# Kernel tuning notes

Hardware: AMD Instinct MI355X
Metric: run time of the kernel (lower is better)

Reference implementation:

```python
import jax, jax.numpy as jnp
import numpy as np

NUM_HEADS = 32
NUM_KV_HEADS = 8
HEAD_DIM = 128
EPS = 1e-6
ROPE_THETA = 10000.0


def setup_inputs() -> dict:
    key = jax.random.key(0)
    k1, k2, k3 = jax.random.split(key, 3)
    B, S, H = 2, 2048, 4096
    qkv_out = (NUM_HEADS + 2 * NUM_KV_HEADS) * HEAD_DIM  # 6144
    return {
        "hidden_states": jax.random.normal(k1, (B, S, H), dtype=jnp.float32),
        "positions": jnp.arange(S, dtype=jnp.int32),
        "wqkv": jax.random.normal(k2, (qkv_out, H), dtype=jnp.float32) * 0.02,
        "q_norm_w": jnp.ones((HEAD_DIM,), dtype=jnp.float32),
        "k_norm_w": jnp.ones((HEAD_DIM,), dtype=jnp.float32),
        "wo": jax.random.normal(k3, (H, H), dtype=jnp.float32) * 0.02,
    }


def _rmsnorm(x, w, eps=EPS):
    # per-head RMSNorm over last dim (head_dim), computed in fp32
    xf = x.astype(jnp.float32)
    var = jnp.mean(xf * xf, axis=-1, keepdims=True)
    return (xf * jax.lax.rsqrt(var + eps) * w).astype(x.dtype)


def _rope(x, positions):
    # NeoX-style half rotation, rotary_dim == head_dim
    d = x.shape[-1]
    half = d // 2
    inv_freq = 1.0 / (ROPE_THETA ** (jnp.arange(0, half, dtype=jnp.float32) * 2.0 / d))
    ang = positions.astype(jnp.float32)[:, None] * inv_freq[None, :]  # [S, half]
    cos = jnp.cos(ang)[None, :, None, :]  # [1,S,1,half]
    sin = jnp.sin(ang)[None, :, None, :]
    x1, x2 = x[..., :half], x[..., half:]
    return jnp.concatenate([x1 * cos - x2 * sin, x2 * cos + x1 * sin], axis=-1)


def reference(hidden_states, positions, wqkv, q_norm_w, k_norm_w, wo):
    B, S, H = hidden_states.shape
    scale = HEAD_DIM ** -0.5
    qkv = jnp.einsum("bsh,oh->bso", hidden_states, wqkv)
    q_size = NUM_HEADS * HEAD_DIM
    kv_size = NUM_KV_HEADS * HEAD_DIM
    q = qkv[..., :q_size].reshape(B, S, NUM_HEADS, HEAD_DIM)
    k = qkv[..., q_size:q_size + kv_size].reshape(B, S, NUM_KV_HEADS, HEAD_DIM)
    v = qkv[..., q_size + kv_size:].reshape(B, S, NUM_KV_HEADS, HEAD_DIM)
    q = _rmsnorm(q, q_norm_w)
    k = _rmsnorm(k, k_norm_w)
    q = _rope(q, positions)
    k = _rope(k, positions)
    # GQA: expand kv heads to query heads
    group = NUM_HEADS // NUM_KV_HEADS
    k = jnp.repeat(k, group, axis=2)  # [B,S,NUM_HEADS,D]
    v = jnp.repeat(v, group, axis=2)
    scores = jnp.einsum("bqhd,bkhd->bhqk", q, k) * scale
    causal = jnp.tril(jnp.ones((S, S), dtype=bool))
    scores = jnp.where(causal[None, None], scores, jnp.finfo(scores.dtype).min)
    probs = jax.nn.softmax(scores, axis=-1)
    attn = jnp.einsum("bhqk,bkhd->bqhd", probs, v).reshape(B, S, NUM_HEADS * HEAD_DIM)
    return jnp.einsum("bsi,oi->bso", attn, wo)
```

## Files before the change

### kernel.cpp

```cpp
#include <hip/hip_runtime.h>
#include <hip/hip_bf16.h>
#include <cstdint>
#include <cstddef>

typedef __hip_bfloat16 bf16;
typedef __attribute__((ext_vector_type(8))) short s8v;
typedef __attribute__((ext_vector_type(4))) float f4v;

#define NH 32
#define NKV 8
#define HD 128
#define BB 2
#define SS 2048
#define HH 4096
#define QKVO 6144
#define MM 4096

__device__ __forceinline__ void gld_lds16(const void* g, void* l) {
    __builtin_amdgcn_global_load_lds(
        (const __attribute__((address_space(1))) void*)g,
        (__attribute__((address_space(3))) void*)l, 16, 0, 0);
}

struct alignas(16) bf16x8s { bf16 v[8]; };
__global__ __launch_bounds__(256) void conv_kernel(const float* __restrict__ in,
                                                   bf16* __restrict__ out, int n8) {
    int i = blockIdx.x * 256 + threadIdx.x;
    if (i >= n8) return;
    const float4* in4 = (const float4*)in;
    float4 a = in4[i * 2];
    float4 b = in4[i * 2 + 1];
    bf16x8s p;
    p.v[0] = __float2bfloat16(a.x); p.v[1] = __float2bfloat16(a.y);
    p.v[2] = __float2bfloat16(a.z); p.v[3] = __float2bfloat16(a.w);
    p.v[4] = __float2bfloat16(b.x); p.v[5] = __float2bfloat16(b.y);
    p.v[6] = __float2bfloat16(b.z); p.v[7] = __float2bfloat16(b.w);
    *(bf16x8s*)(out + (size_t)i * 8) = p;
}

template <typename OutT>
__global__ __launch_bounds__(256) void gemm_bt(const bf16* __restrict__ A,
                                               const bf16* __restrict__ Bm,
                                               OutT* __restrict__ C,
                                               int M, int N, int K) {
    __shared__ bf16 sA[128 * 32];
    __shared__ bf16 sB[128 * 32];
    const int tid = threadIdx.x;
    const int lane = tid & 63;
    const int wave = tid >> 6;
    const int l15 = lane & 15, quad = lane >> 4;
    const int wm = (wave >> 1) * 64, wn = (wave & 1) * 64;
    const int bm = blockIdx.x, bn = blockIdx.y;
    const int row = tid >> 2;
    const int col8 = (tid & 3) * 8;
    const bf16* Ag = A + (size_t)(bm * 128 + row) * K + col8;
    const bf16* Bg = Bm + (size_t)(bn * 128 + row) * K + col8;

    f4v acc[4][4] = {};
    for (int kt = 0; kt < K; kt += 32) {
        __syncthreads();
        gld_lds16(Ag + kt, (char*)sA + tid * 16);
        gld_lds16(Ag + (size_t)64 * K + kt, (char*)sA + 4096 + tid * 16);
        gld_lds16(Bg + kt, (char*)sB + tid * 16);
        gld_lds16(Bg + (size_t)64 * K + kt, (char*)sB + 4096 + tid * 16);
        __syncthreads();
        s8v af[4], bfr[4];
#pragma unroll
        for (int mt = 0; mt < 4; mt++)
            af[mt] = *(const s8v*)(sA + (wm + mt * 16 + l15) * 32 + quad * 8);
#pragma unroll
        for (int nt = 0; nt < 4; nt++)
            bfr[nt] = *(const s8v*)(sB + (wn + nt * 16 + l15) * 32 + quad * 8);
#pragma unroll
        for (int mt = 0; mt < 4; mt++)
#pragma unroll
            for (int nt = 0; nt < 4; nt++)
                acc[mt][nt] = __builtin_amdgcn_mfma_f32_16x16x32_bf16(
                    af[mt], bfr[nt], acc[mt][nt], 0, 0, 0);
    }
#pragma unroll
    for (int mt = 0; mt < 4; mt++)
#pragma unroll
        for (int nt = 0; nt < 4; nt++) {
            int r0 = bm * 128 + wm + mt * 16 + quad * 4;
            int c0 = bn * 128 + wn + nt * 16 + l15;
#pragma unroll
            for (int r = 0; r < 4; r++) {
                float v = acc[mt][nt][r];
                if constexpr (sizeof(OutT) == 2)
                    C[(size_t)(r0 + r) * N + c0] = (OutT)__float2bfloat16(v);
                else
                    C[(size_t)(r0 + r) * N + c0] = (OutT)v;
            }
        }
}

__global__ __launch_bounds__(128) void norm_rope_kernel(
    const bf16* __restrict__ qkv, const int* __restrict__ positions,
    const float* __restrict__ qw, const float* __restrict__ kw,
    bf16* __restrict__ qb, bf16* __restrict__ kb) {
    int rowid = blockIdx.x;
    int head = blockIdx.y;
    int d = threadIdx.x;
    int b = rowid >> 11, s = rowid & 2047;
    bool isq = head < NH;
    int col = isq ? head * HD + d : NH * HD + (head - NH) * HD + d;
    float x = __bfloat162float(qkv[(size_t)rowid * QKVO + col]);

    __shared__ float sv[128];
    __shared__ float partial[2];
    float ss = x * x;
#pragma unroll
    for (int off = 32; off; off >>= 1) ss += __shfl_xor(ss, off, 64);
    if ((threadIdx.x & 63) == 0) partial[threadIdx.x >> 6] = ss;
    __syncthreads();
    float var = (partial[0] + partial[1]) * (1.0f / 128.0f);
    float w = isq ? qw[d] : kw[d];
    float xn = x * rsqrtf(var + 1e-6f) * w;
    sv[d] = xn;
    __syncthreads();

    float pos = (float)positions[s];
    float o;
    if (d < 64) {
        float ang = pos * exp2f(-(float)d * 0.20762051f);
        float c, si; __sincosf(ang, &si, &c);
        o = xn * c - sv[d + 64] * si;
    } else {
        int i = d - 64;
        float ang = pos * exp2f(-(float)i * 0.20762051f);
        float c, si; __sincosf(ang, &si, &c);
        o = xn * c + sv[i] * si;
    }
    if (isq) o *= 0.08838834764831845f;
    size_t oidx;
    if (isq) oidx = (((size_t)(b * NH + head) * SS + s) * HD + d);
    else     oidx = (((size_t)(b * NKV + (head - NH)) * SS + s) * HD + d);
    (isq ? qb : kb)[oidx] = __float2bfloat16(o);
}

__global__ __launch_bounds__(256) void vtrans_kernel(const bf16* __restrict__ qkv,
                                                     bf16* __restrict__ vt) {
    int bh = blockIdx.z;
    int s0 = blockIdx.x * 32, d0 = blockIdx.y * 32;
    int b = bh >> 3, hv = bh & 7;
    __shared__ bf16 tile[32][33];
    int tx = threadIdx.x, ty = threadIdx.y;
    size_t colbase = (size_t)(NH + NKV) * HD + hv * HD + d0;
    for (int i = 0; i < 4; i++) {
        int s = s0 + ty + i * 8;
        tile[ty + i * 8][tx] = qkv[(size_t)(b * SS + s) * QKVO + colbase + tx];
    }
    __syncthreads();
    for (int i = 0; i < 4; i++) {
        int d = d0 + ty + i * 8;
        vt[((size_t)(bh * HD + d)) * SS + s0 + tx] = tile[tx][ty + i * 8];
    }
}

__global__ __launch_bounds__(512, 4) void attn_kernel(
    const bf16* __restrict__ q, const bf16* __restrict__ k,
    const bf16* __restrict__ vt, bf16* __restrict__ out) {
    int pi = blockIdx.x;
    int h = blockIdx.y;
    int b = blockIdx.z;
    int hk = h >> 2;
    int tid = threadIdx.x, lane = tid & 63, wave = tid >> 6;
    int l15 = lane & 15, quad = lane >> 4;

    __shared__ bf16 sK[64][136];
    __shared__ bf16 sVt[128][72];
    __shared__ bf16 sP[8][16][72];

    const bf16* qg = q + ((size_t)(b * NH + h) * SS) * HD;
    const bf16* kg = k + ((size_t)(b * NKV + hk) * SS) * HD;
    const bf16* vg = vt + ((size_t)(b * NKV + hk) * HD) * SS;

    for (int half = 0; half < 2; half++) {
        int qt = half ? (15 - pi) : pi;
        int q0 = qt * 128;
        int qrow = q0 + wave * 16 + l15;
        s8v qf[4];
#pragma unroll
        for (int kc = 0; kc < 4; kc++)
            qf[kc] = *(const s8v*)(qg + (size_t)qrow * HD + kc * 32 + quad * 8);

        f4v o[8] = {};
        float lp[4] = {0.f, 0.f, 0.f, 0.f};
        int qgrow[4];
#pragma unroll
        for (int r = 0; r < 4; r++) qgrow[r] = q0 + wave * 16 + quad * 4 + r;

        int nkt = 2 * qt + 2;
        for (int kt = 0; kt < nkt; kt++) {
            int kbase = kt * 64;
            __syncthreads();
#pragma unroll
            for (int it = 0; it < 2; it++) {
                int c = tid + it * 512;
                int r = c >> 4, c8 = (c & 15) * 8;
                *(float4*)(&sK[r][c8]) =
                    *(const float4*)(kg + (size_t)(kbase + r) * HD + c8);
            }
#pragma unroll
            for (int it = 0; it < 2; it++) {
                int c = tid + it * 512;
                int dr = c >> 3, ck = (c & 7) * 8;
                *(float4*)(&sVt[dr][ck]) =
                    *(const float4*)(vg + (size_t)dr * SS + kbase + ck);
            }
            __syncthreads();

            f4v sc[4];
#pragma unroll
            for (int nt = 0; nt < 4; nt++) {
                f4v a = {0.f, 0.f, 0.f, 0.f};
#pragma unroll
                for (int kc = 0; kc < 4; kc++) {
                    s8v bfrag = *(const s8v*)(&sK[nt * 16 + l15][kc * 32 + quad * 8]);
                    a = __builtin_amdgcn_mfma_f32_16x16x32_bf16(qf[kc], bfrag, a, 0, 0, 0);
                }
                sc[nt] = a;
            }
#pragma unroll
            for (int nt = 0; nt < 4; nt++) {
                int kcol = kbase + nt * 16 + l15;
#pragma unroll
                for (int r = 0; r < 4; r++) {
                    float pv = (kcol > qgrow[r]) ? 0.f : __expf(sc[nt][r]);
                    sc[nt][r] = pv;
                    lp[r] += pv;
                }
            }
#pragma unroll
            for (int nt = 0; nt < 4; nt++)
#pragma unroll
                for (int r = 0; r < 4; r++)
                    sP[wave][quad * 4 + r][nt * 16 + l15] = __float2bfloat16(sc[nt][r]);
            asm volatile("s_waitcnt lgkmcnt(0)" ::: "memory");
            s8v pa[2];
#pragma unroll
            for (int kc = 0; kc < 2; kc++)
                pa[kc] = *(const s8v*)(&sP[wave][l15][kc * 32 + quad * 8]);
#pragma unroll
            for (int dt = 0; dt < 8; dt++)
#pragma unroll
                for (int kc = 0; kc < 2; kc++) {
                    s8v vb = *(const s8v*)(&sVt[dt * 16 + l15][kc * 32 + quad * 8]);
                    o[dt] = __builtin_amdgcn_mfma_f32_16x16x32_bf16(pa[kc], vb, o[dt], 0, 0, 0);
                }
        }
#pragma unroll
        for (int off = 1; off < 16; off <<= 1)
#pragma unroll
            for (int r = 0; r < 4; r++) lp[r] += __shfl_xor(lp[r], off, 64);
#pragma unroll
        for (int r = 0; r < 4; r++) {
            float inv = 1.0f / lp[r];
            int sg = qgrow[r];
#pragma unroll
            for (int dt = 0; dt < 8; dt++) {
                int d = dt * 16 + l15;
                out[(((size_t)(b * SS + sg)) * NH + h) * HD + d] =
                    __float2bfloat16(o[dt][r] * inv);
            }
        }
    }
}

extern "C" void kernel_launch(void* const* d_in, const int* in_sizes, int n_in,
                              void* d_out, int out_size, void* d_ws, size_t ws_size,
                              hipStream_t stream) {
    const float* hidden = (const float*)d_in[0];
    const int* positions = (const int*)d_in[1];
    const float* wqkv = (const float*)d_in[2];
    const float* qnw = (const float*)d_in[3];
    const float* knw = (const float*)d_in[4];
    const float* wo = (const float*)d_in[5];
    float* out = (float*)d_out;

    char* ws = (char*)d_ws;
    bf16* hid_bf = (bf16*)ws;
    bf16* wbuf   = (bf16*)(ws + 33554432);
    bf16* qkv    = (bf16*)(ws + 33554432 + 50331648);
    bf16* qb     = (bf16*)(ws + 33554432 + 50331648 + 50331648);
    bf16* kb     = (bf16*)(ws + 33554432 + 50331648 + 50331648 + 33554432);
    bf16* vtb    = (bf16*)(ws + 33554432 + 50331648 + 50331648 + 33554432 + 8388608);
    bf16* attn   = qkv;

    conv_kernel<<<2097152 / 256, 256, 0, stream>>>(hidden, hid_bf, 2097152);
    conv_kernel<<<3145728 / 256, 256, 0, stream>>>(wqkv, wbuf, 3145728);
    gemm_bt<bf16><<<dim3(32, 48), 256, 0, stream>>>(hid_bf, wbuf, qkv, MM, QKVO, HH);
    norm_rope_kernel<<<dim3(4096, 40), 128, 0, stream>>>(qkv, positions, qnw, knw, qb, kb);
    vtrans_kernel<<<dim3(64, 4, 16), dim3(32, 8), 0, stream>>>(qkv, vtb);
    attn_kernel<<<dim3(8, 32, 2), 512, 0, stream>>>(qb, kb, vtb, attn);
    conv_kernel<<<2097152 / 256, 256, 0, stream>>>(wo, wbuf, 2097152);
    gemm_bt<float><<<dim3(32, 32), 256, 0, stream>>>(attn, wbuf, out, MM, HH, HH);
}
```

Before: 864.2 us.

## Replace GEMM with 256x256 double-buffered swizzled-LDS pipelined MFMA kernel

Replaces the simple 128x128 single-buffered GEMM with a 256x256-tile, 512-thread kernel. It uses double-buffered LDS, XOR-swizzled shared layout, split-phase async global-to-LDS staging interleaved with MFMA blocks, s_setprio, and workgroup index swizzling for L2 locality. The goal is to hide load latency, raise arithmetic intensity, and cut LDS bank conflicts in both projection GEMMs. In exchange it uses 128KB of LDS and many more registers, and the hand-placed waitcnt counts are fragile.

```diff
diff --git a/kernel.cpp b/kernel.cpp
--- a/kernel.cpp
+++ b/kernel.cpp
@@ -21,6 +21,8 @@
         (const __attribute__((address_space(1))) void*)g,
         (__attribute__((address_space(3))) void*)l, 16, 0, 0);
 }
+
+#define MFMA_BF16(a, b, c) __builtin_amdgcn_mfma_f32_16x16x32_bf16((a), (b), (c), 0, 0, 0)
 
 struct alignas(16) bf16x8s { bf16 v[8]; };
 __global__ __launch_bounds__(256) void conv_kernel(const float* __restrict__ in,
@@ -38,55 +40,139 @@
     *(bf16x8s*)(out + (size_t)i * 8) = p;
 }
 
+__device__ __forceinline__ void stage_half(const bf16* __restrict__ gbase, int ldg,
+                                           int kt, int h, bf16* lbase, int tid) {
+    int srow = tid >> 3;
+    int slot = (tid & 7) ^ (srow & 7);
+    const bf16* g = gbase + (size_t)(h * 128 + srow) * ldg + (size_t)kt * 64 + slot * 8;
+    char* l = (char*)lbase + h * 16384 + tid * 16;
+    gld_lds16(g, l);
+    gld_lds16(g + (size_t)64 * ldg, l + 8192);
+}
+
 template <typename OutT>
-__global__ __launch_bounds__(256) void gemm_bt(const bf16* __restrict__ A,
-                                               const bf16* __restrict__ Bm,
-                                               OutT* __restrict__ C,
-                                               int M, int N, int K) {
-    __shared__ bf16 sA[128 * 32];
-    __shared__ bf16 sB[128 * 32];
+__global__ __launch_bounds__(512, 2) void gemm_bt256(const bf16* __restrict__ A,
+                                                     const bf16* __restrict__ Bm,
+                                                     OutT* __restrict__ C,
+                                                     int M, int N, int K) {
+    __shared__ bf16 sA[2][256 * 64];
+    __shared__ bf16 sB[2][256 * 64];
     const int tid = threadIdx.x;
     const int lane = tid & 63;
     const int wave = tid >> 6;
     const int l15 = lane & 15, quad = lane >> 4;
-    const int wm = (wave >> 1) * 64, wn = (wave & 1) * 64;
-    const int bm = blockIdx.x, bn = blockIdx.y;
-    const int row = tid >> 2;
-    const int col8 = (tid & 3) * 8;
-    const bf16* Ag = A + (size_t)(bm * 128 + row) * K + col8;
-    const bf16* Bg = Bm + (size_t)(bn * 128 + row) * K + col8;
-
-    f4v acc[4][4] = {};
-    for (int kt = 0; kt < K; kt += 32) {
-        __syncthreads();
-        gld_lds16(Ag + kt, (char*)sA + tid * 16);
-        gld_lds16(Ag + (size_t)64 * K + kt, (char*)sA + 4096 + tid * 16);
-        gld_lds16(Bg + kt, (char*)sB + tid * 16);
-        gld_lds16(Bg + (size_t)64 * K + kt, (char*)sB + 4096 + tid * 16);
-        __syncthreads();
-        s8v af[4], bfr[4];
-#pragma unroll
-        for (int mt = 0; mt < 4; mt++)
-            af[mt] = *(const s8v*)(sA + (wm + mt * 16 + l15) * 32 + quad * 8);
-#pragma unroll
-        for (int nt = 0; nt < 4; nt++)
-            bfr[nt] = *(const s8v*)(sB + (wn + nt * 16 + l15) * 32 + quad * 8);
-#pragma unroll
-        for (int mt = 0; mt < 4; mt++)
-#pragma unroll
-            for (int nt = 0; nt < 4; nt++)
-                acc[mt][nt] = __builtin_amdgcn_mfma_f32_16x16x32_bf16(
-                    af[mt], bfr[nt], acc[mt][nt], 0, 0, 0);
-    }
-#pragma unroll
-    for (int mt = 0; mt < 4; mt++)
-#pragma unroll
-        for (int nt = 0; nt < 4; nt++) {
-            int r0 = bm * 128 + wm + mt * 16 + quad * 4;
-            int c0 = bn * 128 + wn + nt * 16 + l15;
-#pragma unroll
-            for (int r = 0; r < 4; r++) {
-                float v = acc[mt][nt][r];
+    const int wm = wave >> 2;
+    const int wn = wave & 3;
+
+    const int nbn = N >> 8;
+    const int nwg = (M >> 8) * nbn;
+    const int orig = blockIdx.y * gridDim.x + blockIdx.x;
+    const int cpx = nwg >> 3;
+    const int swz = (orig & 7) * cpx + (orig >> 3);
+    const int bm = swz / nbn, bn = swz % nbn;
+
+    const bf16* Ab = A + (size_t)bm * 256 * K;
+    const bf16* Bb = Bm + (size_t)bn * 256 * K;
+    const int NT = K >> 6;
+
+    const int soff0 = (quad ^ (l15 & 7)) << 4;
+    const int ra  = (wm * 128 + l15) * 128;
+    const int rbb = (wn * 64 + l15) * 128;
+#define LDA(p, m, k) (*(const s8v*)((const char*)sA[p] + ra  + (m) * 2048 + (soff0 ^ ((k) << 6))))
+#define LDB(p, n, k) (*(const s8v*)((const char*)sB[p] + rbb + (n) * 2048 + (soff0 ^ ((k) << 6))))
+
+    f4v acc[8][4] = {};
+    s8v a[4][2], b0[2][2], b1[2][2];
+
+    stage_half(Bb, K, 0, 0, sB[0], tid);
+    stage_half(Ab, K, 0, 0, sA[0], tid);
+    stage_half(Bb, K, 0, 1, sB[0], tid);
+    stage_half(Ab, K, 0, 1, sA[0], tid);
+    stage_half(Bb, K, 1, 0, sB[1], tid);
+    stage_half(Ab, K, 1, 0, sA[1], tid);
+    asm volatile("s_waitcnt vmcnt(4)" ::: "memory");
+    __builtin_amdgcn_s_barrier();
+
+    for (int t = 0; t < NT; ++t) {
+        const int p = t & 1;
+#pragma unroll
+        for (int m = 0; m < 4; ++m) { a[m][0] = LDA(p, m, 0); a[m][1] = LDA(p, m, 1); }
+#pragma unroll
+        for (int n = 0; n < 2; ++n) { b0[n][0] = LDB(p, n, 0); b0[n][1] = LDB(p, n, 1); }
+        if (t + 1 < NT) stage_half(Bb, K, t + 1, 1, sB[p ^ 1], tid);
+        asm volatile("s_waitcnt lgkmcnt(8)" ::: "memory");
+        __builtin_amdgcn_s_barrier();
+        asm volatile("s_waitcnt lgkmcnt(0)" ::: "memory");
+        __builtin_amdgcn_sched_barrier(0);
+        __builtin_amdgcn_s_setprio(1);
+#pragma unroll
+        for (int m = 0; m < 4; ++m)
+#pragma unroll
+            for (int n = 0; n < 2; ++n) {
+                acc[m][n] = MFMA_BF16(a[m][0], b0[n][0], acc[m][n]);
+                acc[m][n] = MFMA_BF16(a[m][1], b0[n][1], acc[m][n]);
+            }
+        __builtin_amdgcn_s_setprio(0);
+        __builtin_amdgcn_s_barrier();
+#pragma unroll
+        for (int n = 0; n < 2; ++n) { b1[n][0] = LDB(p, n + 2, 0); b1[n][1] = LDB(p, n + 2, 1); }
+        if (t + 1 < NT) stage_half(Ab, K, t + 1, 1, sA[p ^ 1], tid);
+        __builtin_amdgcn_s_barrier();
+        asm volatile("s_waitcnt lgkmcnt(0)" ::: "memory");
+        __builtin_amdgcn_sched_barrier(0);
+        __builtin_amdgcn_s_setprio(1);
+#pragma unroll
+        for (int m = 0; m < 4; ++m)
+#pragma unroll
+            for (int n = 0; n < 2; ++n) {
+                acc[m][n + 2] = MFMA_BF16(a[m][0], b1[n][0], acc[m][n + 2]);
+                acc[m][n + 2] = MFMA_BF16(a[m][1], b1[n][1], acc[m][n + 2]);
+            }
+        __builtin_amdgcn_s_setprio(0);
+        __builtin_amdgcn_s_barrier();
+#pragma unroll
+        for (int m = 0; m < 4; ++m) { a[m][0] = LDA(p, m + 4, 0); a[m][1] = LDA(p, m + 4, 1); }
+        if (t + 2 < NT) stage_half(Bb, K, t + 2, 0, sB[p], tid);
+        __builtin_amdgcn_s_barrier();
+        asm volatile("s_waitcnt lgkmcnt(0)" ::: "memory");
+        __builtin_amdgcn_sched_barrier(0);
+        __builtin_amdgcn_s_setprio(1);
+#pragma unroll
+        for (int m = 0; m < 4; ++m)
+#pragma unroll
+            for (int n = 0; n < 2; ++n) {
+                acc[m + 4][n + 2] = MFMA_BF16(a[m][0], b1[n][0], acc[m + 4][n + 2]);
+                acc[m + 4][n + 2] = MFMA_BF16(a[m][1], b1[n][1], acc[m + 4][n + 2]);
+            }
+        __builtin_amdgcn_s_setprio(0);
+        __builtin_amdgcn_s_barrier();
+        if (t + 2 < NT) stage_half(Ab, K, t + 2, 0, sA[p], tid);
+        __builtin_amdgcn_s_barrier();
+        __builtin_amdgcn_s_setprio(1);
+#pragma unroll
+        for (int m = 0; m < 4; ++m)
+#pragma unroll
+            for (int n = 0; n < 2; ++n) {
+                acc[m + 4][n] = MFMA_BF16(a[m][0], b0[n][0], acc[m + 4][n]);
+                acc[m + 4][n] = MFMA_BF16(a[m][1], b0[n][1], acc[m + 4][n]);
+            }
+        __builtin_amdgcn_s_setprio(0);
+        if (t + 2 < NT) { asm volatile("s_waitcnt vmcnt(4)" ::: "memory"); }
+        else            { asm volatile("s_waitcnt vmcnt(0)" ::: "memory"); }
+        __builtin_amdgcn_s_barrier();
+    }
+#undef LDA
+#undef LDB
+
+#pragma unroll
+    for (int m = 0; m < 8; ++m)
+#pragma unroll
+        for (int n = 0; n < 4; ++n) {
+            int r0 = bm * 256 + wm * 128 + m * 16 + quad * 4;
+            int c0 = bn * 256 + wn * 64 + n * 16 + l15;
+#pragma unroll
+            for (int r = 0; r < 4; ++r) {
+                float v = acc[m][n][r];
                 if constexpr (sizeof(OutT) == 2)
                     C[(size_t)(r0 + r) * N + c0] = (OutT)__float2bfloat16(v);
                 else
@@ -290,10 +376,10 @@
 
     conv_kernel<<<2097152 / 256, 256, 0, stream>>>(hidden, hid_bf, 2097152);
     conv_kernel<<<3145728 / 256, 256, 0, stream>>>(wqkv, wbuf, 3145728);
-    gemm_bt<bf16><<<dim3(32, 48), 256, 0, stream>>>(hid_bf, wbuf, qkv, MM, QKVO, HH);
+    gemm_bt256<bf16><<<dim3(16, 24), 512, 0, stream>>>(hid_bf, wbuf, qkv, MM, QKVO, HH);
     norm_rope_kernel<<<dim3(4096, 40), 128, 0, stream>>>(qkv, positions, qnw, knw, qb, kb);
     vtrans_kernel<<<dim3(64, 4, 16), dim3(32, 8), 0, stream>>>(qkv, vtb);
     attn_kernel<<<dim3(8, 32, 2), 512, 0, stream>>>(qb, kb, vtb, attn);
     conv_kernel<<<2097152 / 256, 256, 0, stream>>>(wo, wbuf, 2097152);
-    gemm_bt<float><<<dim3(32, 32), 256, 0, stream>>>(attn, wbuf, out, MM, HH, HH);
-}
+    gemm_bt256<float><<<dim3(16, 16), 512, 0, stream>>>(attn, wbuf, out, MM, HH, HH);
+}
```

New measurement: 779.2 us. 1.11x faster.

## Replace GEMM with 256x256-tile, 4-stage pipelined, swizzled-LDS MFMA kernel

Applied to the files above, without the earlier changes.

Both projection GEMMs now use a 512-thread kernel with 256x256 output tiles, so each wave computes a 128x64 sub-tile. A 4-slot LDS ring is filled three k-steps ahead with direct global-to-LDS loads, paced by explicit vmcnt waits and one barrier per step. LDS rows use an XOR swizzle to avoid bank conflicts, and the workgroup order is remapped for L2 locality. The goal is to hide global load latency and raise arithmetic intensity, at the cost of 128 KB of LDS per block, heavy register use, and fewer workgroups (384 and 256) spread over the CUs.

```diff
diff --git a/kernel.cpp b/kernel.cpp
--- a/kernel.cpp
+++ b/kernel.cpp
@@ -21,6 +21,8 @@
         (const __attribute__((address_space(1))) void*)g,
         (__attribute__((address_space(3))) void*)l, 16, 0, 0);
 }
+
+#define MFMA_BF16(a, b, c) __builtin_amdgcn_mfma_f32_16x16x32_bf16((a), (b), (c), 0, 0, 0)
 
 struct alignas(16) bf16x8s { bf16 v[8]; };
 __global__ __launch_bounds__(256) void conv_kernel(const float* __restrict__ in,
@@ -38,55 +40,97 @@
     *(bf16x8s*)(out + (size_t)i * 8) = p;
 }
 
+__device__ __forceinline__ void stageT(const bf16* __restrict__ g, int ldg, int kt,
+                                       int r0, char* lslot, int lane) {
+    int sub = lane >> 2;
+    int row = r0 + sub;
+    int cs = (lane & 3) ^ (sub & 3);
+    gld_lds16(g + (size_t)row * ldg + kt * 32 + cs * 8,
+              lslot + r0 * 64 + lane * 16);
+}
+
 template <typename OutT>
-__global__ __launch_bounds__(256) void gemm_bt(const bf16* __restrict__ A,
-                                               const bf16* __restrict__ Bm,
-                                               OutT* __restrict__ C,
-                                               int M, int N, int K) {
-    __shared__ bf16 sA[128 * 32];
-    __shared__ bf16 sB[128 * 32];
+__global__ __launch_bounds__(512, 2) void gemm_bt256(const bf16* __restrict__ A,
+                                                     const bf16* __restrict__ Bm,
+                                                     OutT* __restrict__ C,
+                                                     int M, int N, int K) {
+    __shared__ bf16 sA[4][256 * 32];
+    __shared__ bf16 sB[4][256 * 32];
     const int tid = threadIdx.x;
     const int lane = tid & 63;
     const int wave = tid >> 6;
     const int l15 = lane & 15, quad = lane >> 4;
-    const int wm = (wave >> 1) * 64, wn = (wave & 1) * 64;
-    const int bm = blockIdx.x, bn = blockIdx.y;
-    const int row = tid >> 2;
-    const int col8 = (tid & 3) * 8;
-    const bf16* Ag = A + (size_t)(bm * 128 + row) * K + col8;
-    const bf16* Bg = Bm + (size_t)(bn * 128 + row) * K + col8;
-
-    f4v acc[4][4] = {};
-    for (int kt = 0; kt < K; kt += 32) {
-        __syncthreads();
-        gld_lds16(Ag + kt, (char*)sA + tid * 16);
-        gld_lds16(Ag + (size_t)64 * K + kt, (char*)sA + 4096 + tid * 16);
-        gld_lds16(Bg + kt, (char*)sB + tid * 16);
-        gld_lds16(Bg + (size_t)64 * K + kt, (char*)sB + 4096 + tid * 16);
-        __syncthreads();
-        s8v af[4], bfr[4];
-#pragma unroll
-        for (int mt = 0; mt < 4; mt++)
-            af[mt] = *(const s8v*)(sA + (wm + mt * 16 + l15) * 32 + quad * 8);
-#pragma unroll
-        for (int nt = 0; nt < 4; nt++)
-            bfr[nt] = *(const s8v*)(sB + (wn + nt * 16 + l15) * 32 + quad * 8);
-#pragma unroll
-        for (int mt = 0; mt < 4; mt++)
-#pragma unroll
-            for (int nt = 0; nt < 4; nt++)
-                acc[mt][nt] = __builtin_amdgcn_mfma_f32_16x16x32_bf16(
-                    af[mt], bfr[nt], acc[mt][nt], 0, 0, 0);
-    }
-#pragma unroll
-    for (int mt = 0; mt < 4; mt++)
-#pragma unroll
-        for (int nt = 0; nt < 4; nt++) {
-            int r0 = bm * 128 + wm + mt * 16 + quad * 4;
-            int c0 = bn * 128 + wn + nt * 16 + l15;
-#pragma unroll
-            for (int r = 0; r < 4; r++) {
-                float v = acc[mt][nt][r];
+    const int wm = wave >> 2;
+    const int wn = wave & 3;
+
+    const int nbn = N >> 8;
+    const int nwg = (M >> 8) * nbn;
+    const int orig = blockIdx.y * gridDim.x + blockIdx.x;
+    const int cpx = nwg >> 3;
+    const int swz = (orig & 7) * cpx + (orig >> 3);
+    const int bm = swz / nbn, bn = swz % nbn;
+
+    const bf16* Ab = A + (size_t)bm * 256 * K;
+    const bf16* Bb = Bm + (size_t)bn * 256 * K;
+    const int NT = K >> 5;
+
+    const int soff  = (quad ^ (l15 & 3)) << 4;
+    const int raoff = (wm * 128 + l15) * 64 + soff;
+    const int rboff = (wn * 64 + l15) * 64 + soff;
+    const int sr0 = wave * 32;
+
+    f4v acc[8][4] = {};
+
+#pragma unroll
+    for (int u = 0; u < 3; ++u) {
+        stageT(Ab, K, u, sr0,      (char*)sA[u], lane);
+        stageT(Ab, K, u, sr0 + 16, (char*)sA[u], lane);
+        stageT(Bb, K, u, sr0,      (char*)sB[u], lane);
+        stageT(Bb, K, u, sr0 + 16, (char*)sB[u], lane);
+    }
+    asm volatile("s_waitcnt vmcnt(8)" ::: "memory");
+    __builtin_amdgcn_s_barrier();
+
+    for (int t = 0; t < NT; ++t) {
+        const int sl = t & 3;
+        const char* pA = (const char*)sA[sl];
+        const char* pB = (const char*)sB[sl];
+        s8v a[8], b[4];
+#pragma unroll
+        for (int m = 0; m < 8; ++m) a[m] = *(const s8v*)(pA + raoff + m * 1024);
+#pragma unroll
+        for (int n = 0; n < 4; ++n) b[n] = *(const s8v*)(pB + rboff + n * 1024);
+        if (t + 3 < NT) {
+            const int kt = t + 3, ds = kt & 3;
+            stageT(Ab, K, kt, sr0,      (char*)sA[ds], lane);
+            stageT(Ab, K, kt, sr0 + 16, (char*)sA[ds], lane);
+            stageT(Bb, K, kt, sr0,      (char*)sB[ds], lane);
+            stageT(Bb, K, kt, sr0 + 16, (char*)sB[ds], lane);
+        }
+        asm volatile("s_waitcnt lgkmcnt(0)" ::: "memory");
+        __builtin_amdgcn_sched_barrier(0);
+        __builtin_amdgcn_s_setprio(1);
+#pragma unroll
+        for (int m = 0; m < 8; ++m)
+#pragma unroll
+            for (int n = 0; n < 4; ++n)
+                acc[m][n] = MFMA_BF16(a[m], b[n], acc[m][n]);
+        __builtin_amdgcn_s_setprio(0);
+        if (t + 3 < NT)      { asm volatile("s_waitcnt vmcnt(8)" ::: "memory"); }
+        else if (t + 3 == NT){ asm volatile("s_waitcnt vmcnt(4)" ::: "memory"); }
+        else if (t + 2 == NT){ asm volatile("s_waitcnt vmcnt(0)" ::: "memory"); }
+        if (t + 1 < NT) __builtin_amdgcn_s_barrier();
+    }
+
+#pragma unroll
+    for (int m = 0; m < 8; ++m)
+#pragma unroll
+        for (int n = 0; n < 4; ++n) {
+            int r0 = bm * 256 + wm * 128 + m * 16 + quad * 4;
+            int c0 = bn * 256 + wn * 64 + n * 16 + l15;
+#pragma unroll
+            for (int r = 0; r < 4; ++r) {
+                float v = acc[m][n][r];
                 if constexpr (sizeof(OutT) == 2)
                     C[(size_t)(r0 + r) * N + c0] = (OutT)__float2bfloat16(v);
                 else
@@ -290,10 +334,10 @@
 
     conv_kernel<<<2097152 / 256, 256, 0, stream>>>(hidden, hid_bf, 2097152);
     conv_kernel<<<3145728 / 256, 256, 0, stream>>>(wqkv, wbuf, 3145728);
-    gemm_bt<bf16><<<dim3(32, 48), 256, 0, stream>>>(hid_bf, wbuf, qkv, MM, QKVO, HH);
+    gemm_bt256<bf16><<<dim3(16, 24), 512, 0, stream>>>(hid_bf, wbuf, qkv, MM, QKVO, HH);
     norm_rope_kernel<<<dim3(4096, 40), 128, 0, stream>>>(qkv, positions, qnw, knw, qb, kb);
     vtrans_kernel<<<dim3(64, 4, 16), dim3(32, 8), 0, stream>>>(qkv, vtb);
     attn_kernel<<<dim3(8, 32, 2), 512, 0, stream>>>(qb, kb, vtb, attn);
     conv_kernel<<<2097152 / 256, 256, 0, stream>>>(wo, wbuf, 2097152);
-    gemm_bt<float><<<dim3(32, 32), 256, 0, stream>>>(attn, wbuf, out, MM, HH, HH);
-}
+    gemm_bt256<float><<<dim3(16, 16), 512, 0, stream>>>(attn, wbuf, out, MM, HH, HH);
+}
```

Result: faster. 771.9 us (-10.7%).
